# Optimization experiments

Measured on AMD Instinct MI355X. Metric: run time of the kernel, lower is better.

Reference implementation:

```python
import math
import jax, jax.numpy as jnp
import numpy as np

NUM_HEADS = 8
FACTOR = 5


def setup_inputs() -> dict:
    key = jax.random.key(0)
    ks = jax.random.split(key, 8)
    B, N, C = 8, 4096, 512
    s = 0.02
    x = jax.random.normal(ks[0], (B, N, C), dtype=jnp.float32)
    Wq = jax.random.normal(ks[1], (C, C), dtype=jnp.float32) * s
    Wk = jax.random.normal(ks[2], (C, C), dtype=jnp.float32) * s
    Wv = jax.random.normal(ks[3], (C, C), dtype=jnp.float32) * s
    Wp = jax.random.normal(ks[4], (C, C), dtype=jnp.float32) * s
    bq = jnp.zeros((C,), jnp.float32)
    bk = jnp.zeros((C,), jnp.float32)
    bv = jnp.zeros((C,), jnp.float32)
    bp = jnp.zeros((C,), jnp.float32)
    sample_k = min(FACTOR * int(np.ceil(np.log(N))), N)  # 45
    index_sample = jax.random.randint(ks[5], (N, sample_k), 0, N, dtype=jnp.int64)
    return {"x": x, "Wq": Wq, "bq": bq, "Wk": Wk, "bk": bk,
            "Wv": Wv, "bv": bv, "Wp": Wp, "bp": bp,
            "index_sample": index_sample}


def reference(x, Wq, bq, Wk, bk, Wv, bv, Wp, bp, index_sample):
    B, N, C = x.shape
    H = NUM_HEADS
    Dh = C // H
    L_Q = L_K = N
    # qkv projections (torch Linear: x @ W.T + b; W sampled symmetric so use x @ W + b)
    q = (x @ Wq + bq).reshape(B, N, H, Dh).transpose(0, 2, 1, 3)  # [B,H,L,Dh]
    k = (x @ Wk + bk).reshape(B, N, H, Dh).transpose(0, 2, 1, 3)
    v = (x @ Wv + bv).reshape(B, N, H, Dh).transpose(0, 2, 1, 3)

    u = min(FACTOR * int(np.ceil(np.log(L_Q))), L_Q)  # n_top
    scale = (C // H) ** (-0.5)

    # _prob_QK: sampled scores per query
    K_sample = k[:, :, index_sample, :]                       # [B,H,L_Q,s,Dh]
    QK_sample = jnp.einsum('bhld,bhlsd->bhls', q, K_sample)   # [B,H,L_Q,s]
    M = QK_sample.max(axis=-1) - QK_sample.sum(axis=-1) / L_K # sparsity measure
    _, M_top = jax.lax.top_k(M, u)                            # [B,H,u]
    Q_reduce = jnp.take_along_axis(q, M_top[..., None], axis=2)  # [B,H,u,Dh]
    scores = jnp.einsum('bhud,bhkd->bhuk', Q_reduce, k) * scale  # [B,H,u,L_K]

    # initial context: mean of V over keys (mask_flag=False)
    context = jnp.broadcast_to(v.mean(axis=2, keepdims=True), (B, H, L_Q, Dh))

    # update context at selected queries
    attn = jax.nn.softmax(scores, axis=-1)
    out_u = jnp.einsum('bhuk,bhkd->bhud', attn, v)            # [B,H,u,Dh]
    bI = jnp.arange(B)[:, None, None]
    hI = jnp.arange(H)[None, :, None]
    context = context.at[bI, hI, M_top].set(out_u)            # [B,H,L_Q,Dh]

    # mix=True: reshape [B,H,N,Dh] -> [B,N,H*Dh] directly (faithful to source)
    context = context.reshape(B, N, H * Dh)
    return context @ Wp + bp
```

## Files before the change

### kernel.cpp

```cpp
#include <hip/hip_runtime.h>
#include <float.h>

typedef unsigned short ushort_t;
typedef short bf16x8 __attribute__((ext_vector_type(8)));
typedef _Float16 f16x8 __attribute__((ext_vector_type(8)));
typedef float f32x4 __attribute__((ext_vector_type(4)));

#define NS 4096
#define ND 64
#define NU 45
#define NUP 48

__device__ __forceinline__ float bf2f(ushort_t u){ return __uint_as_float(((unsigned)u)<<16); }
__device__ __forceinline__ ushort_t f2bf(float f){
  unsigned u = __float_as_uint(f);
  u += 0x7fffu + ((u>>16)&1u);
  return (ushort_t)(u>>16);
}
__device__ __forceinline__ ushort_t f2h(float f){ _Float16 h=(_Float16)f; return __builtin_bit_cast(ushort_t, h); }
__device__ __forceinline__ float h2f(ushort_t u){ return (float)__builtin_bit_cast(_Float16, u); }

__global__ __launch_bounds__(256) void k_wsplit(const float* __restrict__ Wq,
                                                const float* __restrict__ Wk,
                                                const float* __restrict__ Wv,
                                                ushort_t* __restrict__ wh,
                                                ushort_t* __restrict__ wl)
{
  __shared__ float tile[64][65];
  const int blk = blockIdx.x;
  const int mat = blk >> 6;
  const int kt = (blk >> 3) & 7, nt = blk & 7;
  const float* W = (mat == 0) ? Wq : (mat == 1 ? Wk : Wv);
  const int t = threadIdx.x;
  const int rr = t >> 6, cc = t & 63;
  #pragma unroll
  for (int i = 0; i < 16; i++)
    tile[rr*16 + i][cc] = W[(size_t)(kt*64 + rr*16 + i)*512 + nt*64 + cc];
  __syncthreads();
  #pragma unroll
  for (int i = 0; i < 16; i++) {
    const int n = rr*16 + i;
    const float v = tile[cc][n];
    const ushort_t h = f2bf(v);
    const size_t o = (size_t)(mat*512 + nt*64 + n)*512 + kt*64 + cc;
    wh[o] = h;
    wl[o] = f2bf(v - bf2f(h));
  }
}

__global__ __launch_bounds__(256) void k_xsplit(const float* __restrict__ x,
                                                ushort_t* __restrict__ xh,
                                                ushort_t* __restrict__ xl)
{
  int i = (blockIdx.x*256 + threadIdx.x)*4;
  float4 v = *(const float4*)(x + i);
  ushort4 h, lo;
  h.x = f2bf(v.x); lo.x = f2bf(v.x - bf2f(h.x));
  h.y = f2bf(v.y); lo.y = f2bf(v.y - bf2f(h.y));
  h.z = f2bf(v.z); lo.z = f2bf(v.z - bf2f(h.z));
  h.w = f2bf(v.w); lo.w = f2bf(v.w - bf2f(h.w));
  *(ushort4*)(xh + i) = h;
  *(ushort4*)(xl + i) = lo;
}

template<int MODE>
__global__ __launch_bounds__(256) void k_gemm(
    const ushort_t* __restrict__ xh, const ushort_t* __restrict__ xl,
    const ushort_t* __restrict__ wh, const ushort_t* __restrict__ wl,
    const float* __restrict__ bq, const float* __restrict__ bk, const float* __restrict__ bv,
    float* __restrict__ kf, ushort_t* __restrict__ vfT,
    ushort_t* __restrict__ kb16, ushort_t* __restrict__ qb16)
{
  __shared__ __align__(16) ushort_t smem[20480];
  ushort_t* Ah = smem;
  ushort_t* Al = smem + 5120;
  ushort_t* Bh = smem + (MODE == 1 ? 10240 : 5120);
  ushort_t* Bl = smem + 15360;
  const int nbx = (MODE == 0) ? 4 : 8;
  const int p = blockIdx.y * nbx + blockIdx.x;
  const int cx = p & 7;
  const int local = p >> 3;
  const int by = cx*32 + local/nbx;
  const int bx = local % nbx;
  const int rowbase = by * 128;
  const int colbase = (MODE == 0 ? 0 : 512) + bx*128;
  const int mat = colbase >> 9;
  const int t = threadIdx.x;
  const int l = t & 63;
  const int w = t >> 6;
  const int wm = w >> 1, wn = w & 1;
  f32x4 acc[4][4] = {};
  const int r0 = t >> 2;
  const int c0 = (t & 3) * 8;

  for (int k0 = 0; k0 < 512; k0 += 32) {
    __syncthreads();
    #pragma unroll
    for (int half = 0; half < 2; half++) {
      const int r = r0 + half*64;
      *(uint4*)(&Ah[r*40 + c0]) = *(const uint4*)(&xh[(size_t)(rowbase + r)*512 + k0 + c0]);
      if (MODE == 1) *(uint4*)(&Al[r*40 + c0]) = *(const uint4*)(&xl[(size_t)(rowbase + r)*512 + k0 + c0]);
      *(uint4*)(&Bh[r*40 + c0]) = *(const uint4*)(&wh[(size_t)(colbase + r)*512 + k0 + c0]);
      if (MODE == 1) *(uint4*)(&Bl[r*40 + c0]) = *(const uint4*)(&wl[(size_t)(colbase + r)*512 + k0 + c0]);
    }
    __syncthreads();
    bf16x8 ah[4], al[4], bh8[4], bl8[4];
    #pragma unroll
    for (int m = 0; m < 4; m++) {
      const int off = (wm*64 + m*16 + (l & 15))*40 + (l >> 4)*8;
      ah[m] = *(const bf16x8*)(&Ah[off]);
      if (MODE == 1) al[m] = *(const bf16x8*)(&Al[off]);
    }
    #pragma unroll
    for (int n = 0; n < 4; n++) {
      const int off = (wn*64 + n*16 + (l & 15))*40 + (l >> 4)*8;
      bh8[n] = *(const bf16x8*)(&Bh[off]);
      if (MODE == 1) bl8[n] = *(const bf16x8*)(&Bl[off]);
    }
    #pragma unroll
    for (int m = 0; m < 4; m++)
      #pragma unroll
      for (int n = 0; n < 4; n++) {
        acc[m][n] = __builtin_amdgcn_mfma_f32_16x16x32_bf16(ah[m], bh8[n], acc[m][n], 0, 0, 0);
        if (MODE == 1) {
          acc[m][n] = __builtin_amdgcn_mfma_f32_16x16x32_bf16(ah[m], bl8[n], acc[m][n], 0, 0, 0);
          acc[m][n] = __builtin_amdgcn_mfma_f32_16x16x32_bf16(al[m], bh8[n], acc[m][n], 0, 0, 0);
        }
      }
  }

  if (MODE == 1 && mat == 2) {
    __syncthreads();
    #pragma unroll
    for (int n = 0; n < 4; n++) {
      const int wi_l = wn*64 + n*16 + (l & 15);
      const float bias = bv[(colbase & 511) + wi_l];
      #pragma unroll
      for (int m = 0; m < 4; m++) {
        const int nr_l = wm*64 + m*16 + ((l >> 4) << 2);
        ushort4 pk;
        pk.x = f2h(acc[m][n][0] + bias);
        pk.y = f2h(acc[m][n][1] + bias);
        pk.z = f2h(acc[m][n][2] + bias);
        pk.w = f2h(acc[m][n][3] + bias);
        *(ushort4*)(&smem[wi_l*136 + nr_l]) = pk;
      }
    }
    __syncthreads();
    const int wi2 = t >> 1, half = t & 1;
    const int cim = (colbase & 511) + wi2;
    const int hh2 = cim >> 6, d2 = cim & 63;
    const int b2 = rowbase >> 12;
    const int nr2 = (rowbase & 4095) + half*64;
    ushort_t* op = &vfT[((size_t)(b2*8 + hh2)*ND + d2)*NS + nr2];
    const ushort_t* ip = &smem[wi2*136 + half*64];
    #pragma unroll
    for (int cch = 0; cch < 8; cch++)
      *(uint4*)(op + cch*8) = *(const uint4*)(ip + cch*8);
    return;
  }

  if (MODE == 1) {
    #pragma unroll
    for (int n = 0; n < 4; n++) {
      const int wi = (colbase & 511) + wn*64 + n*16 + (l & 15);
      const int hh = wi >> 6, d = wi & 63;
      const float bias = bk[wi];
      #pragma unroll
      for (int m = 0; m < 4; m++) {
        const int rb = rowbase + wm*64 + m*16 + ((l >> 4) << 2);
        const int b  = rb >> 12, nr = rb & 4095;
        #pragma unroll
        for (int j = 0; j < 4; j++)
          kf[((size_t)(b*8 + hh)*NS + nr + j)*ND + d] = acc[m][n][j] + bias;
      }
    }
  }
  {
    ushort_t* obuf = (MODE == 0) ? qb16 : kb16;
    const float* bias_p = (MODE == 0) ? bq : bk;
    __syncthreads();
    #pragma unroll
    for (int n = 0; n < 4; n++) {
      const int c_l = wn*64 + n*16 + (l & 15);
      const float bias = bias_p[(colbase & 511) + c_l];
      #pragma unroll
      for (int m = 0; m < 4; m++) {
        const int rb_l = wm*64 + m*16 + ((l >> 4) << 2);
        #pragma unroll
        for (int j = 0; j < 4; j++)
          smem[(rb_l + j)*136 + c_l] = f2bf(acc[m][n][j] + bias);
      }
    }
    __syncthreads();
    const int r2 = t >> 1, half = t & 1;
    const int hh2 = ((colbase & 511) >> 6) + half;
    const int b2 = rowbase >> 12;
    const int nr2 = rowbase & 4095;
    ushort_t* op = &obuf[((size_t)(b2*8 + hh2)*NS + nr2 + r2)*ND];
    const ushort_t* ip = &smem[r2*136 + half*64];
    #pragma unroll
    for (int cch = 0; cch < 8; cch++)
      *(uint4*)(op + cch*8) = *(const uint4*)(ip + cch*8);
  }
}

__global__ __launch_bounds__(256) void k_m_approx(const ushort_t* __restrict__ qb16,
                                                  const ushort_t* __restrict__ kb16,
                                                  const int* __restrict__ idxs,
                                                  float* __restrict__ Mv)
{
  __shared__ float qs[4][64];
  __shared__ int   sidx[4][48];
  const int orig = blockIdx.y * 1024 + blockIdx.x;
  const int lin  = (orig & 7) * 8192 + (orig >> 3);
  const int bh   = lin >> 10;
  const int lc   = lin & 1023;
  const int t = threadIdx.x;
  const int wv = t >> 6, lane = t & 63;
  const int l = lc*4 + wv;
  qs[wv][lane] = bf2f(qb16[((size_t)bh*NS + l)*ND + lane]);
  for (int e = t; e < 4*NU; e += 256)
    sidx[e/NU][e%NU] = idxs[(size_t)(lc*4 + e/NU)*NU + e%NU];
  __syncthreads();
  const int g  = lane >> 3;
  const int dq = lane & 7;
  const float* qp = &qs[wv][dq*8];
  int ids[6];
  #pragma unroll
  for (int p = 0; p < 6; p++) {
    const int s = p*8 + g;
    ids[p] = sidx[wv][(s < NU) ? s : NU-1];
  }
  uint4 ku[6];
  #pragma unroll
  for (int p = 0; p < 6; p++)
    ku[p] = *(const uint4*)(&kb16[((size_t)bh*NS + ids[p])*ND + dq*8]);
  float mx = -FLT_MAX, sm = 0.f;
  #pragma unroll
  for (int p = 0; p < 6; p++) {
    const int s = p*8 + g;
    const bool val = (s < NU);
    const ushort_t* kp = (const ushort_t*)&ku[p];
    float p_dot = qp[0]*bf2f(kp[0]) + qp[1]*bf2f(kp[1]) + qp[2]*bf2f(kp[2]) + qp[3]*bf2f(kp[3])
                + qp[4]*bf2f(kp[4]) + qp[5]*bf2f(kp[5]) + qp[6]*bf2f(kp[6]) + qp[7]*bf2f(kp[7]);
    p_dot += __shfl_xor(p_dot, 1, 64);
    p_dot += __shfl_xor(p_dot, 2, 64);
    p_dot += __shfl_xor(p_dot, 4, 64);
    if (val) { mx = fmaxf(mx, p_dot); sm += p_dot; }
  }
  #pragma unroll
  for (int o = 8; o < 64; o <<= 1) {
    mx = fmaxf(mx, __shfl_xor(mx, o, 64));
    sm += __shfl_xor(sm, o, 64);
  }
  if (lane == 0) Mv[bh*NS + l] = mx - sm * (1.0f/(float)NS);
}

template<int NSEL, int OST>
__global__ __launch_bounds__(256) void k_topk(const float* __restrict__ Mv, int* __restrict__ dst)
{
  __shared__ float wvs[4];
  __shared__ int   wis[4];
  const int bh = blockIdx.x, t = threadIdx.x;
  const int wv = t >> 6, lane = t & 63;
  float v[16];
  #pragma unroll
  for (int j = 0; j < 16; j++) v[j] = Mv[bh*NS + j*256 + t];
  unsigned removed = 0;
  float tmax = -FLT_MAX; int tidx = 0x7fffffff;
  #pragma unroll
  for (int j = 0; j < 16; j++) {
    if (v[j] > tmax) { tmax = v[j]; tidx = j*256 + t; }
  }
  for (int it = 0; it < NSEL; it++) {
    float mv = tmax; int mi = tidx;
    #pragma unroll
    for (int o = 1; o < 64; o <<= 1) {
      float vo = __shfl_xor(mv, o, 64); int io = __shfl_xor(mi, o, 64);
      if (vo > mv || (vo == mv && io < mi)) { mv = vo; mi = io; }
    }
    if (lane == 0) { wvs[wv] = mv; wis[wv] = mi; }
    __syncthreads();
    float gv = wvs[0]; int gi = wis[0];
    #pragma unroll
    for (int k2 = 1; k2 < 4; k2++) {
      float vo = wvs[k2]; int io = wis[k2];
      if (vo > gv || (vo == gv && io < gi)) { gv = vo; gi = io; }
    }
    if (t == 0) dst[bh*OST + it] = gi;
    if ((gi & 255) == t) {
      removed |= 1u << (gi >> 8);
      tmax = -FLT_MAX; tidx = 0x7fffffff;
      #pragma unroll
      for (int j = 0; j < 16; j++) {
        bool ok = ((removed >> j) & 1u) == 0u;
        if (ok && (v[j] > tmax || (v[j] == tmax && (j*256+t) < tidx))) { tmax = v[j]; tidx = j*256 + t; }
      }
    }
    __syncthreads();
  }
}

__global__ __launch_bounds__(256) void k_qexact(const float* __restrict__ x,
                                                const ushort_t* __restrict__ wh,
                                                const ushort_t* __restrict__ wl,
                                                const float* __restrict__ bq,
                                                const int* __restrict__ Cand,
                                                float* __restrict__ qex)
{
  const int bh = blockIdx.x, t = threadIdx.x;
  const int wv = t >> 6, l = t & 63;
  const int b = bh >> 3, h = bh & 7;
  const int cand = 16*wv + (l & 15);
  const int n = Cand[bh*64 + cand];
  const float* xr = x + ((size_t)b*NS + n)*512 + (l >> 4)*8;
  f32x4 acc[4] = {};
  for (int k0 = 0; k0 < 512; k0 += 32) {
    float4 v0 = *(const float4*)(xr + k0);
    float4 v1 = *(const float4*)(xr + k0 + 4);
    ushort_t hi[8], lo[8];
    float vv[8] = {v0.x,v0.y,v0.z,v0.w,v1.x,v1.y,v1.z,v1.w};
    #pragma unroll
    for (int j = 0; j < 8; j++) {
      hi[j] = f2bf(vv[j]);
      lo[j] = f2bf(vv[j] - bf2f(hi[j]));
    }
    bf16x8 ah = *(const bf16x8*)hi;
    bf16x8 al = *(const bf16x8*)lo;
    #pragma unroll
    for (int nt = 0; nt < 4; nt++) {
      const size_t boff = (size_t)(h*64 + nt*16 + (l & 15))*512 + k0 + (l >> 4)*8;
      bf16x8 bh8 = *(const bf16x8*)(&wh[boff]);
      bf16x8 bl8 = *(const bf16x8*)(&wl[boff]);
      acc[nt] = __builtin_amdgcn_mfma_f32_16x16x32_bf16(ah, bh8, acc[nt], 0, 0, 0);
      acc[nt] = __builtin_amdgcn_mfma_f32_16x16x32_bf16(ah, bl8, acc[nt], 0, 0, 0);
      acc[nt] = __builtin_amdgcn_mfma_f32_16x16x32_bf16(al, bh8, acc[nt], 0, 0, 0);
    }
  }
  #pragma unroll
  for (int nt = 0; nt < 4; nt++)
    #pragma unroll
    for (int j = 0; j < 4; j++) {
      const int cand_o = 16*wv + (l >> 4)*4 + j;
      const int d_o = nt*16 + (l & 15);
      qex[((size_t)bh*64 + cand_o)*ND + d_o] = acc[nt][j] + bq[h*64 + d_o];
    }
}

__global__ __launch_bounds__(256) void k_mexact(const float* __restrict__ qex,
                                                const float* __restrict__ kf,
                                                const int* __restrict__ idxs,
                                                const int* __restrict__ Cand,
                                                float* __restrict__ Mex)
{
  const int bh = blockIdx.y, qtr = blockIdx.x, t = threadIdx.x;
  const int c = qtr*16 + (t >> 4);
  const int dl = t & 15;
  const int l = Cand[bh*64 + c];
  const float4 q4 = *(const float4*)(&qex[((size_t)bh*64 + c)*ND + dl*4]);
  const float* kbase = kf + (size_t)bh*NS*ND;
  const int* ib = idxs + (size_t)l*NU;
  float mx = -FLT_MAX, sm = 0.f;
  for (int s = 0; s < NU; s++) {
    const int id = ib[s];
    const float4 k4 = *(const float4*)(&kbase[(size_t)id*ND + dl*4]);
    float p = q4.x*k4.x + q4.y*k4.y + q4.z*k4.z + q4.w*k4.w;
    p += __shfl_xor(p, 1, 64);
    p += __shfl_xor(p, 2, 64);
    p += __shfl_xor(p, 4, 64);
    p += __shfl_xor(p, 8, 64);
    mx = fmaxf(mx, p);
    sm += p;
  }
  if (dl == 0) Mex[bh*64 + c] = mx - sm * (1.0f/(float)NS);
}

__global__ void k_sel45(const float* __restrict__ Mex, const int* __restrict__ Cand,
                        int* __restrict__ Mtop, int* __restrict__ MtopSlot)
{
  const int bh = blockIdx.x, lane = threadIdx.x;
  float val = Mex[bh*64 + lane];
  const int n = Cand[bh*64 + lane];
  const int slot = lane;
  for (int it = 0; it < NU; it++) {
    float wv = val; int wn = n; int ws = slot;
    #pragma unroll
    for (int o = 1; o < 64; o <<= 1) {
      float vo = __shfl_xor(wv, o, 64); int io = __shfl_xor(wn, o, 64); int so = __shfl_xor(ws, o, 64);
      if (vo > wv || (vo == wv && io < wn)) { wv = vo; wn = io; ws = so; }
    }
    if (lane == 0) { Mtop[bh*NUP + it] = wn; MtopSlot[bh*NUP + it] = ws; }
    if (n == wn) val = -FLT_MAX;
  }
}

__global__ __launch_bounds__(256) void k_qreduce(const float* __restrict__ qex,
                                                 const int* __restrict__ MtopSlot,
                                                 ushort_t* __restrict__ Qr)
{
  const int bh = blockIdx.x, t = threadIdx.x;
  for (int e = t; e < NUP*ND; e += 256) {
    const int u = e >> 6, d = e & 63;
    float v = 0.f;
    if (u < NU) { const int s = MtopSlot[bh*NUP + u]; v = qex[((size_t)bh*64 + s)*ND + d]; }
    Qr[bh*NUP*ND + e] = f2bf(v * 0.125f);
  }
}

__global__ __launch_bounds__(256) void k_flash(const ushort_t* __restrict__ Qr,
                                               const ushort_t* __restrict__ kb16,
                                               const ushort_t* __restrict__ vfT,
                                               float* __restrict__ Opart,
                                               float* __restrict__ mpart,
                                               float* __restrict__ lpart)
{
  __shared__ __align__(16) ushort_t Plds[3][16][68];
  const int blk = blockIdx.x;
  const int bh = blk & 63, seg = blk >> 6;
  const int t = threadIdx.x, w = t >> 6, l = t & 63;
  if (w >= 3) return;
  const int row0 = w*16;
  bf16x8 aq[2];
  #pragma unroll
  for (int ks = 0; ks < 2; ks++)
    aq[ks] = *(const bf16x8*)(&Qr[((size_t)bh*NUP + row0 + (l & 15))*ND + ks*32 + (l >> 4)*8]);
  f32x4 o[4] = {};
  float m[4], ls[4];
  #pragma unroll
  for (int j = 0; j < 4; j++) { m[j] = -FLT_MAX; ls[j] = 0.f; }
  const int nbeg = seg*512;
  for (int nc = nbeg; nc < nbeg + 512; nc += 64) {
    f32x4 S[4];
    #pragma unroll
    for (int ct = 0; ct < 4; ct++) {
      f32x4 z = {};
      #pragma unroll
      for (int ks = 0; ks < 2; ks++) {
        bf16x8 bk8 = *(const bf16x8*)(&kb16[((size_t)bh*NS + nc + ct*16 + (l & 15))*ND + ks*32 + (l >> 4)*8]);
        z = __builtin_amdgcn_mfma_f32_16x16x32_bf16(aq[ks], bk8, z, 0, 0, 0);
      }
      S[ct] = z;
    }
    float mx[4];
    #pragma unroll
    for (int j = 0; j < 4; j++)
      mx[j] = fmaxf(fmaxf(S[0][j], S[1][j]), fmaxf(S[2][j], S[3][j]));
    #pragma unroll
    for (int o2 = 1; o2 < 16; o2 <<= 1)
      #pragma unroll
      for (int j = 0; j < 4; j++)
        mx[j] = fmaxf(mx[j], __shfl_xor(mx[j], o2, 64));
    float c[4];
    #pragma unroll
    for (int j = 0; j < 4; j++) {
      const float mn = fmaxf(m[j], mx[j]);
      c[j] = __expf(m[j] - mn);
      m[j] = mn;
      ls[j] *= c[j];
    }
    #pragma unroll
    for (int dt = 0; dt < 4; dt++)
      #pragma unroll
      for (int j = 0; j < 4; j++)
        o[dt][j] *= c[j];
    #pragma unroll
    for (int ct = 0; ct < 4; ct++)
      #pragma unroll
      for (int j = 0; j < 4; j++) {
        const float pv = __expf(S[ct][j] - m[j]);
        ls[j] += pv;
        Plds[w][(l >> 4)*4 + j][ct*16 + (l & 15)] = f2h(pv);
      }
    #pragma unroll
    for (int ks2 = 0; ks2 < 2; ks2++) {
      f16x8 ap = __builtin_bit_cast(f16x8, *(const uint4*)(&Plds[w][l & 15][ks2*32 + (l >> 4)*8]));
      #pragma unroll
      for (int dt = 0; dt < 4; dt++) {
        f16x8 bv8 = __builtin_bit_cast(f16x8, *(const uint4*)(&vfT[((size_t)bh*ND + dt*16 + (l & 15))*NS + nc + ks2*32 + (l >> 4)*8]));
        o[dt] = __builtin_amdgcn_mfma_f32_16x16x32_f16(ap, bv8, o[dt], 0, 0, 0);
      }
    }
  }
  #pragma unroll
  for (int o2 = 1; o2 < 16; o2 <<= 1)
    #pragma unroll
    for (int j = 0; j < 4; j++)
      ls[j] += __shfl_xor(ls[j], o2, 64);
  #pragma unroll
  for (int dt = 0; dt < 4; dt++)
    #pragma unroll
    for (int j = 0; j < 4; j++)
      Opart[(((size_t)bh*8 + seg)*NUP + row0 + (l >> 4)*4 + j)*ND + dt*16 + (l & 15)] = o[dt][j];
  if ((l & 15) == 0) {
    #pragma unroll
    for (int j = 0; j < 4; j++) {
      mpart[((size_t)bh*8 + seg)*NUP + row0 + (l >> 4)*4 + j] = m[j];
      lpart[((size_t)bh*8 + seg)*NUP + row0 + (l >> 4)*4 + j] = ls[j];
    }
  }
}

__global__ __launch_bounds__(256) void k_combine(const float* __restrict__ Opart,
                                                 const float* __restrict__ mpart,
                                                 const float* __restrict__ lpart,
                                                 const float* __restrict__ vmean,
                                                 float* __restrict__ delta)
{
  const int bh = blockIdx.x, t = threadIdx.x;
  for (int e = t; e < NUP*ND; e += 256) {
    const int u = e >> 6, d = e & 63;
    float mg = -FLT_MAX;
    #pragma unroll
    for (int s = 0; s < 8; s++) mg = fmaxf(mg, mpart[((size_t)bh*8 + s)*NUP + u]);
    float On = 0.f, Ln = 0.f;
    #pragma unroll
    for (int s = 0; s < 8; s++) {
      const float wgt = __expf(mpart[((size_t)bh*8 + s)*NUP + u] - mg);
      On += wgt * Opart[(((size_t)bh*8 + s)*NUP + u)*ND + d];
      Ln += wgt * lpart[((size_t)bh*8 + s)*NUP + u];
    }
    delta[((size_t)bh*NUP + u)*ND + d] = On/Ln - vmean[bh*ND + d];
  }
}

__global__ __launch_bounds__(256) void k_vmean(const ushort_t* __restrict__ vfT, float* __restrict__ vmean)
{
  __shared__ float red[256];
  const int d = blockIdx.x, bh = blockIdx.y, t = threadIdx.x;
  const ushort_t* vr = vfT + ((size_t)bh*ND + d)*NS;
  float s = 0.f;
  for (int n = t; n < NS; n += 256) s += h2f(vr[n]);
  red[t] = s; __syncthreads();
  for (int st = 128; st > 0; st >>= 1) { if (t < st) red[t] += red[t+st]; __syncthreads(); }
  if (t == 0) vmean[bh*ND + d] = red[0] * (1.0f/(float)NS);
}

__global__ __launch_bounds__(256) void k_uidx_init(int* __restrict__ uidx)
{
  uidx[blockIdx.x*256 + threadIdx.x] = -1;
}

__global__ void k_scatter(const int* __restrict__ Mtop, int* __restrict__ uidx)
{
  const int bh = blockIdx.x, t = threadIdx.x;
  if (t < NU) {
    const int n = Mtop[bh*NUP + t];
    const int b = bh >> 3, h = bh & 7;
    const int nprime = h*512 + (n >> 3);
    uidx[((size_t)b*NS + nprime)*8 + (n & 7)] = bh*NUP + t;
  }
}

__global__ __launch_bounds__(256) void k_corr(const float* __restrict__ delta,
                                              const float* __restrict__ Wp,
                                              const int* __restrict__ Mtop,
                                              float* __restrict__ corr)
{
  __shared__ float dl[64];
  const int bh = blockIdx.y, u = blockIdx.x, t = threadIdx.x;
  const int n = Mtop[bh*NUP + u];
  const int j = n & 7;
  if (t < 64) dl[t] = delta[((size_t)bh*NUP + u)*ND + t];
  __syncthreads();
  for (int c = t; c < 512; c += 256) {
    float s = 0.f;
    #pragma unroll 8
    for (int d2 = 0; d2 < 64; d2++) s += dl[d2] * Wp[(size_t)(j*64 + d2)*512 + c];
    corr[((size_t)bh*NUP + u)*512 + c] = s;
  }
}

__global__ __launch_bounds__(256) void k_wpsum(const float* __restrict__ Wp,
                                               float* __restrict__ Wpsum)
{
  int i = blockIdx.x*256 + threadIdx.x;
  int d2 = i >> 9, c = i & 511;
  float s = 0.f;
  #pragma unroll
  for (int j = 0; j < 8; j++) s += Wp[(size_t)(j*64 + d2)*512 + c];
  Wpsum[i] = s;
}

__global__ __launch_bounds__(256) void k_base(const float* __restrict__ vmean,
                                              const float* __restrict__ Wpsum,
                                              const float* __restrict__ bp,
                                              float* __restrict__ basep)
{
  __shared__ float vm[64];
  const int bh = blockIdx.x, t = threadIdx.x;
  if (t < 64) vm[t] = vmean[bh*ND + t];
  __syncthreads();
  for (int c = t; c < 512; c += 256) {
    float s = bp[c];
    #pragma unroll 8
    for (int d2 = 0; d2 < 64; d2++) s += vm[d2] * Wpsum[d2*512 + c];
    basep[bh*512 + c] = s;
  }
}

__global__ __launch_bounds__(256) void k_assemble(const float* __restrict__ basep,
                                                  const float* __restrict__ corr,
                                                  const int* __restrict__ uidx,
                                                  float* __restrict__ out)
{
  const int b = blockIdx.y, nprime = blockIdx.x, t = threadIdx.x;
  const int h = nprime >> 9;
  const int* ui = uidx + ((size_t)b*NS + nprime)*8;
  float v0 = basep[(b*8 + h)*512 + t];
  float v1 = basep[(b*8 + h)*512 + 256 + t];
  #pragma unroll
  for (int j = 0; j < 8; j++) {
    const int id = ui[j];
    if (id >= 0) { v0 += corr[(size_t)id*512 + t]; v1 += corr[(size_t)id*512 + 256 + t]; }
  }
  const size_t o = ((size_t)b*NS + nprime)*512;
  out[o + t]       = v0;
  out[o + 256 + t] = v1;
}

extern "C" void kernel_launch(void* const* d_in, const int* in_sizes, int n_in,
                              void* d_out, int out_size, void* d_ws, size_t ws_size,
                              hipStream_t stream)
{
  (void)in_sizes; (void)n_in; (void)out_size; (void)ws_size;
  const float* x  = (const float*)d_in[0];
  const float* Wq = (const float*)d_in[1];
  const float* bq = (const float*)d_in[2];
  const float* Wk = (const float*)d_in[3];
  const float* bk = (const float*)d_in[4];
  const float* Wv = (const float*)d_in[5];
  const float* bv = (const float*)d_in[6];
  const float* Wp = (const float*)d_in[7];
  const float* bp = (const float*)d_in[8];
  const int* idxs = (const int*)d_in[9];
  float* out      = (float*)d_out;

  char* w = (char*)d_ws;
  float*    kf    = (float*)(w);
  ushort_t* vfT   = (ushort_t*)(w + 67108864);
  ushort_t* kb16  = (ushort_t*)(w + 100663296);
  ushort_t* xh    = (ushort_t*)(w + 134217728);
  ushort_t* xl    = (ushort_t*)(w + 167772160);
  ushort_t* qb16  = (ushort_t*)(w + 167772160);
  ushort_t* wh    = (ushort_t*)(w + 201326592);
  ushort_t* wl    = (ushort_t*)(w + 202899456);
  float*    Mv    = (float*)(w + 204472320);
  float*    qex   = (float*)(w + 204472320);
  int*      Mtop  = (int*)(w + 205520896);
  int*      MtopSlot = (int*)(w + 205533184);
  int*      Cand  = (int*)(w + 205545472);
  float*    Mex   = (float*)(w + 205561856);
  float*    vmean = (float*)(w + 205578240);
  float*    Wpsum = (float*)(w + 205594624);
  float*    delta  = (float*)(w);
  float*    corr   = (float*)(w + 786432);
  int*      uidx   = (int*)(w + 7077888);
  float*    basep  = (float*)(w + 8126464);
  float*    Opart  = (float*)(w + 8257536);
  float*    mpart  = (float*)(w + 14548992);
  float*    lpart  = (float*)(w + 14647296);
  ushort_t* Qr     = (ushort_t*)(w + 14745600);

  k_wsplit   <<<192, 256, 0, stream>>>(Wq, Wk, Wv, wh, wl);
  k_xsplit   <<<16384, 256, 0, stream>>>(x, xh, xl);
  k_gemm<1>  <<<dim3(8, 256), 256, 0, stream>>>(xh, xl, wh, wl, bq, bk, bv, kf, vfT, kb16, nullptr);
  k_gemm<0>  <<<dim3(4, 256), 256, 0, stream>>>(xh, nullptr, wh, wl, bq, bk, bv, nullptr, nullptr, nullptr, qb16);
  k_wpsum    <<<128, 256, 0, stream>>>(Wp, Wpsum);
  k_m_approx <<<dim3(1024, 64), 256, 0, stream>>>(qb16, kb16, idxs, Mv);
  k_vmean    <<<dim3(64, 64), 256, 0, stream>>>(vfT, vmean);
  k_topk<64,64> <<<64, 256, 0, stream>>>(Mv, Cand);
  k_qexact   <<<64, 256, 0, stream>>>(x, wh, wl, bq, Cand, qex);
  k_mexact   <<<dim3(4, 64), 256, 0, stream>>>(qex, kf, idxs, Cand, Mex);
  k_sel45    <<<64, 64, 0, stream>>>(Mex, Cand, Mtop, MtopSlot);
  k_qreduce  <<<64, 256, 0, stream>>>(qex, MtopSlot, Qr);
  k_flash    <<<512, 256, 0, stream>>>(Qr, kb16, vfT, Opart, mpart, lpart);
  k_combine  <<<64, 256, 0, stream>>>(Opart, mpart, lpart, vmean, delta);
  k_uidx_init<<<1024, 256, 0, stream>>>(uidx);
  k_scatter  <<<64, 64, 0, stream>>>(Mtop, uidx);
  k_corr     <<<dim3(45, 64), 256, 0, stream>>>(delta, Wp, Mtop, corr);
  k_base     <<<64, 256, 0, stream>>>(vmean, Wpsum, bp, basep);
  k_assemble <<<dim3(4096, 8), 256, 0, stream>>>(basep, corr, uidx, out);
}
```

Measured before the change: 547.4 us.

## Merge Q/K/V GEMMs, store K as bf16 hi/lo pair, fuse small kernels

Merges the two GEMM launches into one grid that handles Q (single bf16 pass) and K/V (split-precision) tiles. The fp32 K copy becomes a bf16 hi/lo pair written through shared memory, which halves K's footprint and replaces scattered fp32 stores. Several small kernels are folded together to cut launch overhead: mexact, sel45 and qreduce become one, wpsum moves into wsplit, uidx init into combine, and base into corr. The exact-M pass now rebuilds K from the hi+lo bf16 pair, which can differ slightly from fp32 K and may perturb the top-k selection.

```diff
diff --git a/kernel.cpp b/kernel.cpp
--- a/kernel.cpp
+++ b/kernel.cpp
@@ -23,8 +23,10 @@
 __global__ __launch_bounds__(256) void k_wsplit(const float* __restrict__ Wq,
                                                 const float* __restrict__ Wk,
                                                 const float* __restrict__ Wv,
+                                                const float* __restrict__ Wp,
                                                 ushort_t* __restrict__ wh,
-                                                ushort_t* __restrict__ wl)
+                                                ushort_t* __restrict__ wl,
+                                                float* __restrict__ Wpsum)
 {
   __shared__ float tile[64][65];
   const int blk = blockIdx.x;
@@ -45,6 +47,14 @@
     const size_t o = (size_t)(mat*512 + nt*64 + n)*512 + kt*64 + cc;
     wh[o] = h;
     wl[o] = f2bf(v - bf2f(h));
+  }
+  if (blk < 128) {
+    const int i = blk*256 + t;
+    const int d2 = i >> 9, c = i & 511;
+    float s = 0.f;
+    #pragma unroll
+    for (int j = 0; j < 8; j++) s += Wp[(size_t)(j*64 + d2)*512 + c];
+    Wpsum[i] = s;
   }
 }
 
@@ -63,28 +73,27 @@
   *(ushort4*)(xl + i) = lo;
 }
 
-template<int MODE>
-__global__ __launch_bounds__(256) void k_gemm(
+__global__ __launch_bounds__(256) void k_gemm_all(
     const ushort_t* __restrict__ xh, const ushort_t* __restrict__ xl,
     const ushort_t* __restrict__ wh, const ushort_t* __restrict__ wl,
     const float* __restrict__ bq, const float* __restrict__ bk, const float* __restrict__ bv,
-    float* __restrict__ kf, ushort_t* __restrict__ vfT,
-    ushort_t* __restrict__ kb16, ushort_t* __restrict__ qb16)
+    ushort_t* __restrict__ vfT, ushort_t* __restrict__ kb16,
+    ushort_t* __restrict__ kl16, ushort_t* __restrict__ qb16)
 {
   __shared__ __align__(16) ushort_t smem[20480];
+  const int p = blockIdx.y * 12 + blockIdx.x;
+  const int cx = p & 7;
+  const int local = p >> 3;
+  const int by = cx*32 + local/12;
+  const int bx = local % 12;
+  const bool isQ = (bx >= 8);
+  const int rowbase = by * 128;
+  const int colbase = isQ ? (bx - 8)*128 : 512 + bx*128;
+  const int mat = colbase >> 9;
   ushort_t* Ah = smem;
   ushort_t* Al = smem + 5120;
-  ushort_t* Bh = smem + (MODE == 1 ? 10240 : 5120);
+  ushort_t* Bh = smem + (isQ ? 5120 : 10240);
   ushort_t* Bl = smem + 15360;
-  const int nbx = (MODE == 0) ? 4 : 8;
-  const int p = blockIdx.y * nbx + blockIdx.x;
-  const int cx = p & 7;
-  const int local = p >> 3;
-  const int by = cx*32 + local/nbx;
-  const int bx = local % nbx;
-  const int rowbase = by * 128;
-  const int colbase = (MODE == 0 ? 0 : 512) + bx*128;
-  const int mat = colbase >> 9;
   const int t = threadIdx.x;
   const int l = t & 63;
   const int w = t >> 6;
@@ -99,9 +108,9 @@
     for (int half = 0; half < 2; half++) {
       const int r = r0 + half*64;
       *(uint4*)(&Ah[r*40 + c0]) = *(const uint4*)(&xh[(size_t)(rowbase + r)*512 + k0 + c0]);
-      if (MODE == 1) *(uint4*)(&Al[r*40 + c0]) = *(const uint4*)(&xl[(size_t)(rowbase + r)*512 + k0 + c0]);
+      if (!isQ) *(uint4*)(&Al[r*40 + c0]) = *(const uint4*)(&xl[(size_t)(rowbase + r)*512 + k0 + c0]);
       *(uint4*)(&Bh[r*40 + c0]) = *(const uint4*)(&wh[(size_t)(colbase + r)*512 + k0 + c0]);
-      if (MODE == 1) *(uint4*)(&Bl[r*40 + c0]) = *(const uint4*)(&wl[(size_t)(colbase + r)*512 + k0 + c0]);
+      if (!isQ) *(uint4*)(&Bl[r*40 + c0]) = *(const uint4*)(&wl[(size_t)(colbase + r)*512 + k0 + c0]);
     }
     __syncthreads();
     bf16x8 ah[4], al[4], bh8[4], bl8[4];
@@ -109,27 +118,27 @@
     for (int m = 0; m < 4; m++) {
       const int off = (wm*64 + m*16 + (l & 15))*40 + (l >> 4)*8;
       ah[m] = *(const bf16x8*)(&Ah[off]);
-      if (MODE == 1) al[m] = *(const bf16x8*)(&Al[off]);
+      if (!isQ) al[m] = *(const bf16x8*)(&Al[off]);
     }
     #pragma unroll
     for (int n = 0; n < 4; n++) {
       const int off = (wn*64 + n*16 + (l & 15))*40 + (l >> 4)*8;
       bh8[n] = *(const bf16x8*)(&Bh[off]);
-      if (MODE == 1) bl8[n] = *(const bf16x8*)(&Bl[off]);
+      if (!isQ) bl8[n] = *(const bf16x8*)(&Bl[off]);
     }
     #pragma unroll
     for (int m = 0; m < 4; m++)
       #pragma unroll
       for (int n = 0; n < 4; n++) {
         acc[m][n] = __builtin_amdgcn_mfma_f32_16x16x32_bf16(ah[m], bh8[n], acc[m][n], 0, 0, 0);
-        if (MODE == 1) {
+        if (!isQ) {
           acc[m][n] = __builtin_amdgcn_mfma_f32_16x16x32_bf16(ah[m], bl8[n], acc[m][n], 0, 0, 0);
           acc[m][n] = __builtin_amdgcn_mfma_f32_16x16x32_bf16(al[m], bh8[n], acc[m][n], 0, 0, 0);
         }
       }
   }
 
-  if (MODE == 1 && mat == 2) {
+  if (mat == 2) {
     __syncthreads();
     #pragma unroll
     for (int n = 0; n < 4; n++) {
@@ -160,25 +169,9 @@
     return;
   }
 
-  if (MODE == 1) {
-    #pragma unroll
-    for (int n = 0; n < 4; n++) {
-      const int wi = (colbase & 511) + wn*64 + n*16 + (l & 15);
-      const int hh = wi >> 6, d = wi & 63;
-      const float bias = bk[wi];
-      #pragma unroll
-      for (int m = 0; m < 4; m++) {
-        const int rb = rowbase + wm*64 + m*16 + ((l >> 4) << 2);
-        const int b  = rb >> 12, nr = rb & 4095;
-        #pragma unroll
-        for (int j = 0; j < 4; j++)
-          kf[((size_t)(b*8 + hh)*NS + nr + j)*ND + d] = acc[m][n][j] + bias;
-      }
-    }
-  }
-  {
-    ushort_t* obuf = (MODE == 0) ? qb16 : kb16;
-    const float* bias_p = (MODE == 0) ? bq : bk;
+  const float* bias_p = isQ ? bq : bk;
+  const int npass = isQ ? 1 : 2;
+  for (int pass = 0; pass < npass; pass++) {
     __syncthreads();
     #pragma unroll
     for (int n = 0; n < 4; n++) {
@@ -188,11 +181,15 @@
       for (int m = 0; m < 4; m++) {
         const int rb_l = wm*64 + m*16 + ((l >> 4) << 2);
         #pragma unroll
-        for (int j = 0; j < 4; j++)
-          smem[(rb_l + j)*136 + c_l] = f2bf(acc[m][n][j] + bias);
-      }
-    }
-    __syncthreads();
+        for (int j = 0; j < 4; j++) {
+          const float val = acc[m][n][j] + bias;
+          const ushort_t h = f2bf(val);
+          smem[(rb_l + j)*136 + c_l] = (pass == 0) ? h : f2bf(val - bf2f(h));
+        }
+      }
+    }
+    __syncthreads();
+    ushort_t* obuf = isQ ? qb16 : (pass == 0 ? kb16 : kl16);
     const int r2 = t >> 1, half = t & 1;
     const int hh2 = ((colbase & 511) >> 6) + half;
     const int b2 = rowbase >> 12;
@@ -348,62 +345,61 @@
     }
 }
 
-__global__ __launch_bounds__(256) void k_mexact(const float* __restrict__ qex,
-                                                const float* __restrict__ kf,
-                                                const int* __restrict__ idxs,
-                                                const int* __restrict__ Cand,
-                                                float* __restrict__ Mex)
-{
-  const int bh = blockIdx.y, qtr = blockIdx.x, t = threadIdx.x;
-  const int c = qtr*16 + (t >> 4);
+__global__ __launch_bounds__(256) void k_msel(const float* __restrict__ qex,
+                                              const ushort_t* __restrict__ kb16,
+                                              const ushort_t* __restrict__ kl16,
+                                              const int* __restrict__ idxs,
+                                              const int* __restrict__ Cand,
+                                              int* __restrict__ Mtop,
+                                              ushort_t* __restrict__ Qr)
+{
+  __shared__ float MexL[64];
+  __shared__ int   MslotL[NU];
+  const int bh = blockIdx.x, t = threadIdx.x;
   const int dl = t & 15;
-  const int l = Cand[bh*64 + c];
-  const float4 q4 = *(const float4*)(&qex[((size_t)bh*64 + c)*ND + dl*4]);
-  const float* kbase = kf + (size_t)bh*NS*ND;
-  const int* ib = idxs + (size_t)l*NU;
-  float mx = -FLT_MAX, sm = 0.f;
-  for (int s = 0; s < NU; s++) {
-    const int id = ib[s];
-    const float4 k4 = *(const float4*)(&kbase[(size_t)id*ND + dl*4]);
-    float p = q4.x*k4.x + q4.y*k4.y + q4.z*k4.z + q4.w*k4.w;
-    p += __shfl_xor(p, 1, 64);
-    p += __shfl_xor(p, 2, 64);
-    p += __shfl_xor(p, 4, 64);
-    p += __shfl_xor(p, 8, 64);
-    mx = fmaxf(mx, p);
-    sm += p;
-  }
-  if (dl == 0) Mex[bh*64 + c] = mx - sm * (1.0f/(float)NS);
-}
-
-__global__ void k_sel45(const float* __restrict__ Mex, const int* __restrict__ Cand,
-                        int* __restrict__ Mtop, int* __restrict__ MtopSlot)
-{
-  const int bh = blockIdx.x, lane = threadIdx.x;
-  float val = Mex[bh*64 + lane];
-  const int n = Cand[bh*64 + lane];
-  const int slot = lane;
-  for (int it = 0; it < NU; it++) {
-    float wv = val; int wn = n; int ws = slot;
-    #pragma unroll
-    for (int o = 1; o < 64; o <<= 1) {
-      float vo = __shfl_xor(wv, o, 64); int io = __shfl_xor(wn, o, 64); int so = __shfl_xor(ws, o, 64);
-      if (vo > wv || (vo == wv && io < wn)) { wv = vo; wn = io; ws = so; }
-    }
-    if (lane == 0) { Mtop[bh*NUP + it] = wn; MtopSlot[bh*NUP + it] = ws; }
-    if (n == wn) val = -FLT_MAX;
-  }
-}
-
-__global__ __launch_bounds__(256) void k_qreduce(const float* __restrict__ qex,
-                                                 const int* __restrict__ MtopSlot,
-                                                 ushort_t* __restrict__ Qr)
-{
-  const int bh = blockIdx.x, t = threadIdx.x;
+  for (int qtr = 0; qtr < 4; qtr++) {
+    const int c = qtr*16 + (t >> 4);
+    const int l = Cand[bh*64 + c];
+    const float4 q4 = *(const float4*)(&qex[((size_t)bh*64 + c)*ND + dl*4]);
+    const int* ib = idxs + (size_t)l*NU;
+    float mx = -FLT_MAX, sm = 0.f;
+    for (int s = 0; s < NU; s++) {
+      const int id = ib[s];
+      const size_t ko = ((size_t)bh*NS + id)*ND + dl*4;
+      const ushort4 h4 = *(const ushort4*)(&kb16[ko]);
+      const ushort4 l4 = *(const ushort4*)(&kl16[ko]);
+      float p = q4.x*(bf2f(h4.x)+bf2f(l4.x)) + q4.y*(bf2f(h4.y)+bf2f(l4.y))
+              + q4.z*(bf2f(h4.z)+bf2f(l4.z)) + q4.w*(bf2f(h4.w)+bf2f(l4.w));
+      p += __shfl_xor(p, 1, 64);
+      p += __shfl_xor(p, 2, 64);
+      p += __shfl_xor(p, 4, 64);
+      p += __shfl_xor(p, 8, 64);
+      mx = fmaxf(mx, p);
+      sm += p;
+    }
+    if (dl == 0) MexL[c] = mx - sm * (1.0f/(float)NS);
+  }
+  __syncthreads();
+  if (t < 64) {
+    float val = MexL[t];
+    const int n = Cand[bh*64 + t];
+    const int slot = t;
+    for (int it = 0; it < NU; it++) {
+      float wv = val; int wn = n; int ws = slot;
+      #pragma unroll
+      for (int o = 1; o < 64; o <<= 1) {
+        float vo = __shfl_xor(wv, o, 64); int io = __shfl_xor(wn, o, 64); int so = __shfl_xor(ws, o, 64);
+        if (vo > wv || (vo == wv && io < wn)) { wv = vo; wn = io; ws = so; }
+      }
+      if (t == 0) { Mtop[bh*NUP + it] = wn; MslotL[it] = ws; }
+      if (n == wn) val = -FLT_MAX;
+    }
+  }
+  __syncthreads();
   for (int e = t; e < NUP*ND; e += 256) {
     const int u = e >> 6, d = e & 63;
     float v = 0.f;
-    if (u < NU) { const int s = MtopSlot[bh*NUP + u]; v = qex[((size_t)bh*64 + s)*ND + d]; }
+    if (u < NU) { const int s = MslotL[u]; v = qex[((size_t)bh*64 + s)*ND + d]; }
     Qr[bh*NUP*ND + e] = f2bf(v * 0.125f);
   }
 }
@@ -505,9 +501,13 @@
                                                  const float* __restrict__ mpart,
                                                  const float* __restrict__ lpart,
                                                  const float* __restrict__ vmean,
-                                                 float* __restrict__ delta)
-{
-  const int bh = blockIdx.x, t = threadIdx.x;
+                                                 float* __restrict__ delta,
+                                                 int* __restrict__ uidx)
+{
+  const int blk = blockIdx.x, t = threadIdx.x;
+  uidx[blk*256 + t] = -1;
+  if (blk >= 64) return;
+  const int bh = blk;
   for (int e = t; e < NUP*ND; e += 256) {
     const int u = e >> 6, d = e & 63;
     float mg = -FLT_MAX;
@@ -536,11 +536,6 @@
   if (t == 0) vmean[bh*ND + d] = red[0] * (1.0f/(float)NS);
 }
 
-__global__ __launch_bounds__(256) void k_uidx_init(int* __restrict__ uidx)
-{
-  uidx[blockIdx.x*256 + threadIdx.x] = -1;
-}
-
 __global__ void k_scatter(const int* __restrict__ Mtop, int* __restrict__ uidx)
 {
   const int bh = blockIdx.x, t = threadIdx.x;
@@ -552,13 +547,28 @@
   }
 }
 
-__global__ __launch_bounds__(256) void k_corr(const float* __restrict__ delta,
-                                              const float* __restrict__ Wp,
-                                              const int* __restrict__ Mtop,
-                                              float* __restrict__ corr)
+__global__ __launch_bounds__(256) void k_corrbase(const float* __restrict__ delta,
+                                                  const float* __restrict__ Wp,
+                                                  const int* __restrict__ Mtop,
+                                                  const float* __restrict__ vmean,
+                                                  const float* __restrict__ Wpsum,
+                                                  const float* __restrict__ bp,
+                                                  float* __restrict__ corr,
+                                                  float* __restrict__ basep)
 {
   __shared__ float dl[64];
   const int bh = blockIdx.y, u = blockIdx.x, t = threadIdx.x;
+  if (u == 45) {
+    if (t < 64) dl[t] = vmean[bh*ND + t];
+    __syncthreads();
+    for (int c = t; c < 512; c += 256) {
+      float s = bp[c];
+      #pragma unroll 8
+      for (int d2 = 0; d2 < 64; d2++) s += dl[d2] * Wpsum[d2*512 + c];
+      basep[bh*512 + c] = s;
+    }
+    return;
+  }
   const int n = Mtop[bh*NUP + u];
   const int j = n & 7;
   if (t < 64) dl[t] = delta[((size_t)bh*NUP + u)*ND + t];
@@ -568,34 +578,6 @@
     #pragma unroll 8
     for (int d2 = 0; d2 < 64; d2++) s += dl[d2] * Wp[(size_t)(j*64 + d2)*512 + c];
     corr[((size_t)bh*NUP + u)*512 + c] = s;
-  }
-}
-
-__global__ __launch_bounds__(256) void k_wpsum(const float* __restrict__ Wp,
-                                               float* __restrict__ Wpsum)
-{
-  int i = blockIdx.x*256 + threadIdx.x;
-  int d2 = i >> 9, c = i & 511;
-  float s = 0.f;
-  #pragma unroll
-  for (int j = 0; j < 8; j++) s += Wp[(size_t)(j*64 + d2)*512 + c];
-  Wpsum[i] = s;
-}
-
-__global__ __launch_bounds__(256) void k_base(const float* __restrict__ vmean,
-                                              const float* __restrict__ Wpsum,
-                                              const float* __restrict__ bp,
-                                              float* __restrict__ basep)
-{
-  __shared__ float vm[64];
-  const int bh = blockIdx.x, t = threadIdx.x;
-  if (t < 64) vm[t] = vmean[bh*ND + t];
-  __syncthreads();
-  for (int c = t; c < 512; c += 256) {
-    float s = bp[c];
-    #pragma unroll 8
-    for (int d2 = 0; d2 < 64; d2++) s += vm[d2] * Wpsum[d2*512 + c];
-    basep[bh*512 + c] = s;
   }
 }
 
@@ -637,48 +619,40 @@
   float* out      = (float*)d_out;
 
   char* w = (char*)d_ws;
-  float*    kf    = (float*)(w);
-  ushort_t* vfT   = (ushort_t*)(w + 67108864);
-  ushort_t* kb16  = (ushort_t*)(w + 100663296);
+  ushort_t* vfT   = (ushort_t*)(w);
+  ushort_t* kb16  = (ushort_t*)(w + 33554432);
+  ushort_t* kl16  = (ushort_t*)(w + 67108864);
+  ushort_t* qb16  = (ushort_t*)(w + 100663296);
   ushort_t* xh    = (ushort_t*)(w + 134217728);
   ushort_t* xl    = (ushort_t*)(w + 167772160);
-  ushort_t* qb16  = (ushort_t*)(w + 167772160);
   ushort_t* wh    = (ushort_t*)(w + 201326592);
   ushort_t* wl    = (ushort_t*)(w + 202899456);
   float*    Mv    = (float*)(w + 204472320);
   float*    qex   = (float*)(w + 204472320);
   int*      Mtop  = (int*)(w + 205520896);
-  int*      MtopSlot = (int*)(w + 205533184);
-  int*      Cand  = (int*)(w + 205545472);
-  float*    Mex   = (float*)(w + 205561856);
-  float*    vmean = (float*)(w + 205578240);
-  float*    Wpsum = (float*)(w + 205594624);
-  float*    delta  = (float*)(w);
-  float*    corr   = (float*)(w + 786432);
-  int*      uidx   = (int*)(w + 7077888);
-  float*    basep  = (float*)(w + 8126464);
-  float*    Opart  = (float*)(w + 8257536);
-  float*    mpart  = (float*)(w + 14548992);
-  float*    lpart  = (float*)(w + 14647296);
-  ushort_t* Qr     = (ushort_t*)(w + 14745600);
-
-  k_wsplit   <<<192, 256, 0, stream>>>(Wq, Wk, Wv, wh, wl);
+  int*      Cand  = (int*)(w + 205533184);
+  float*    vmean = (float*)(w + 205549568);
+  float*    Wpsum = (float*)(w + 205565952);
+  float*    delta  = (float*)(w + 134217728);
+  float*    corr   = (float*)(w + 135004160);
+  int*      uidx   = (int*)(w + 141295616);
+  float*    basep  = (float*)(w + 142344192);
+  float*    Opart  = (float*)(w + 142475264);
+  float*    mpart  = (float*)(w + 148766720);
+  float*    lpart  = (float*)(w + 148865024);
+  ushort_t* Qr     = (ushort_t*)(w + 148963328);
+
+  k_wsplit   <<<192, 256, 0, stream>>>(Wq, Wk, Wv, Wp, wh, wl, Wpsum);
   k_xsplit   <<<16384, 256, 0, stream>>>(x, xh, xl);
-  k_gemm<1>  <<<dim3(8, 256), 256, 0, stream>>>(xh, xl, wh, wl, bq, bk, bv, kf, vfT, kb16, nullptr);
-  k_gemm<0>  <<<dim3(4, 256), 256, 0, stream>>>(xh, nullptr, wh, wl, bq, bk, bv, nullptr, nullptr, nullptr, qb16);
-  k_wpsum    <<<128, 256, 0, stream>>>(Wp, Wpsum);
+  k_gemm_all <<<dim3(12, 256), 256, 0, stream>>>(xh, xl, wh, wl, bq, bk, bv, vfT, kb16, kl16, qb16);
   k_m_approx <<<dim3(1024, 64), 256, 0, stream>>>(qb16, kb16, idxs, Mv);
   k_vmean    <<<dim3(64, 64), 256, 0, stream>>>(vfT, vmean);
   k_topk<64,64> <<<64, 256, 0, stream>>>(Mv, Cand);
   k_qexact   <<<64, 256, 0, stream>>>(x, wh, wl, bq, Cand, qex);
-  k_mexact   <<<dim3(4, 64), 256, 0, stream>>>(qex, kf, idxs, Cand, Mex);
-  k_sel45    <<<64, 64, 0, stream>>>(Mex, Cand, Mtop, MtopSlot);
-  k_qreduce  <<<64, 256, 0, stream>>>(qex, MtopSlot, Qr);
+  k_msel     <<<64, 256, 0, stream>>>(qex, kb16, kl16, idxs, Cand, Mtop, Qr);
   k_flash    <<<512, 256, 0, stream>>>(Qr, kb16, vfT, Opart, mpart, lpart);
-  k_combine  <<<64, 256, 0, stream>>>(Opart, mpart, lpart, vmean, delta);
-  k_uidx_init<<<1024, 256, 0, stream>>>(uidx);
+  k_combine  <<<1024, 256, 0, stream>>>(Opart, mpart, lpart, vmean, delta, uidx);
   k_scatter  <<<64, 64, 0, stream>>>(Mtop, uidx);
-  k_corr     <<<dim3(45, 64), 256, 0, stream>>>(delta, Wp, Mtop, corr);
-  k_base     <<<64, 256, 0, stream>>>(vmean, Wpsum, bp, basep);
+  k_corrbase <<<dim3(46, 64), 256, 0, stream>>>(delta, Wp, Mtop, vmean, Wpsum, bp, corr, basep);
   k_assemble <<<dim3(4096, 8), 256, 0, stream>>>(basep, corr, uidx, out);
 }
```

New measurement: 723.2 us. 1.32x slower.
